# Optimization experiments

Measured on AMD Instinct MI355X. Metric: run time of the kernel, lower is better.

The kernel has to match this reference:

```python
import jax, jax.numpy as jnp
import numpy as np

B, N, C_IN, C_OUT, T, K = 16, 128, 64, 128, 256, 9
PAD = (K - 1) // 2


def conv1d(x, w, b, pad):
    # x: (n, c_in, t), w: (c_out, c_in, k) -> (n, c_out, t)
    y = jax.lax.conv_general_dilated(x, w, (1,), [(pad, pad)],
                                     dimension_numbers=('NCH', 'OIH', 'NCH'))
    return y + b[None, :, None]


def setup_inputs() -> dict:
    key = jax.random.key(0)
    ks = jax.random.split(key, 10)
    xav = lambda k, shape, fan_in, fan_out: jax.random.uniform(
        k, shape, jnp.float32, -1.0, 1.0) * np.sqrt(6.0 / (fan_in + fan_out))
    return {
        'x': jax.random.normal(ks[0], (B, N, C_IN, T), jnp.float32),
        'adjacency': jax.random.uniform(ks[1], (B, N, N), jnp.float32),
        'w_t1': xav(ks[2], (C_OUT, C_IN, K), C_IN * K, C_OUT * K),
        'b_t1': jnp.zeros((C_OUT,), jnp.float32),
        'w_sp': xav(ks[3], (C_OUT, C_OUT), C_OUT, C_OUT),
        'b_sp': jnp.zeros((C_OUT,), jnp.float32),
        'w_t2': xav(ks[4], (C_OUT, C_OUT, K), C_OUT * K, C_OUT * K),
        'b_t2': jnp.zeros((C_OUT,), jnp.float32),
        'w_res': xav(ks[5], (C_OUT, C_IN, 1), C_IN, C_OUT),
        'b_res': jnp.zeros((C_OUT,), jnp.float32),
    }


def reference(x, adjacency, w_t1, b_t1, w_sp, b_sp, w_t2, b_t2, w_res, b_res):
    b, n, c_in, t = x.shape
    xr = x.reshape(b * n, c_in, t)
    # temporal1 + relu
    h = jax.nn.relu(conv1d(xr, w_t1, b_t1, PAD))            # (b*n, c_out, t)
    c_out = h.shape[1]
    h = h.reshape(b, n, c_out, t).transpose(0, 3, 1, 2)      # (b, t, n, c)
    # spatial graph conv, batched over all timesteps at once
    support = jnp.einsum('btnc,co->btno', h, w_sp)
    h = jnp.einsum('bnm,btmo->btno', adjacency, support) + b_sp
    h = jax.nn.relu(h)
    h = h.transpose(0, 2, 3, 1).reshape(b * n, c_out, t)     # (b*n, c, t)
    # temporal2
    h = conv1d(h, w_t2, b_t2, PAD)
    # residual 1x1 conv (in_channels != out_channels)
    res = conv1d(xr, w_res, b_res, 0)
    out = (h + res).reshape(b, n, c_out, t)
    # dropout: identity in eval mode
    return out
```

## Files before the change

kernel.cpp:

```cpp
#include <hip/hip_runtime.h>

#define B_ 16
#define N_ 128
#define CI_ 64
#define CO_ 128
#define T_ 256
#define K_ 9

typedef __attribute__((ext_vector_type(8))) __bf16 bf16x8;
typedef __attribute__((ext_vector_type(4))) float f32x4;
typedef __attribute__((ext_vector_type(8))) unsigned short ushort8;

__device__ __forceinline__ unsigned short tobf(float f) {
  return __builtin_bit_cast(unsigned short, (__bf16)f);
}
__device__ __forceinline__ int swzs(int row, int col0) {
  return ((col0 >> 3) ^ (row & 7)) << 3;
}
__device__ __forceinline__ int swz(int row, int col) {
  return (((col >> 3) ^ (row & 7)) << 3) | (col & 7);
}
#define FRAG(p, idx) (*(const bf16x8*)((p) + (size_t)(idx) * 8))

__device__ __forceinline__ void gload16(const void* g, void* l) {
  __builtin_amdgcn_global_load_lds(
      (const __attribute__((address_space(1))) void*)g,
      (__attribute__((address_space(3))) void*)l, 16, 0, 0);
}

__global__ __launch_bounds__(256) void k_prep(
    const float* __restrict__ w1, const float* __restrict__ w2,
    const float* __restrict__ wsp, const float* __restrict__ wr,
    const float* __restrict__ adj,
    unsigned short* __restrict__ w1f, unsigned short* __restrict__ w2f,
    unsigned short* __restrict__ wrf, unsigned short* __restrict__ wspf,
    unsigned short* __restrict__ adjf) {
  int idx = blockIdx.x * 256 + threadIdx.x;
  int stride = gridDim.x * 256;
  for (int i = idx; i < 73728; i += stride) {
    int e = i & 7, lane = (i >> 3) & 63, ni = (i >> 9) & 3, cg = (i >> 11) & 1;
    int kb = (i >> 12) & 1, k = i >> 13;
    int co = cg * 64 + ni * 16 + (lane & 15), ci = kb * 32 + (lane >> 4) * 8 + e;
    w1f[i] = tobf(w1[(co * 64 + ci) * 9 + k]);
  }
  for (int i = idx; i < 147456; i += stride) {
    int e = i & 7, lane = (i >> 3) & 63, ni = (i >> 9) & 3, cg = (i >> 11) & 1;
    int kb = (i >> 12) & 3, k = i >> 14;
    int co = cg * 64 + ni * 16 + (lane & 15), c = kb * 32 + (lane >> 4) * 8 + e;
    w2f[i] = tobf(w2[(co * 128 + c) * 9 + k]);
  }
  for (int i = idx; i < 8192; i += stride) {
    int e = i & 7, lane = (i >> 3) & 63, ni = (i >> 9) & 3, cg = (i >> 11) & 1;
    int kb = i >> 12;
    int co = cg * 64 + ni * 16 + (lane & 15), ci = kb * 32 + (lane >> 4) * 8 + e;
    wrf[i] = tobf(wr[co * 64 + ci]);
  }
  for (int i = idx; i < 16384; i += stride) {
    int e = i & 7, lane = (i >> 3) & 63, mi = (i >> 9) & 3, og = (i >> 11) & 1;
    int kb = i >> 12;
    int o = og * 64 + mi * 16 + (lane & 15), c = kb * 32 + (lane >> 4) * 8 + e;
    wspf[i] = tobf(wsp[c * 128 + o]);
  }
  for (int i = idx; i < 262144; i += stride) {
    int e = i & 7, lane = (i >> 3) & 63, ni = (i >> 9) & 1, ng = (i >> 10) & 3;
    int kb = (i >> 12) & 3, b = i >> 14;
    int nn = ng * 32 + ni * 16 + (lane & 15), m = kb * 32 + (lane >> 4) * 8 + e;
    adjf[i] = tobf(adj[(b * 128 + nn) * 128 + m]);
  }
}

__global__ __launch_bounds__(256, 4) void k_conv1(
    const float* __restrict__ x, const unsigned short* __restrict__ w1f,
    const float* __restrict__ b1, unsigned short* __restrict__ h1,
    unsigned short* __restrict__ xT) {
  __shared__ alignas(16) char smem[17408];
  unsigned short* xs = (unsigned short*)smem;
  unsigned short* ot = (unsigned short*)smem;

  int tid = threadIdx.x, blk = blockIdx.x;
  int bn = blk >> 1, th = blk & 1, t0 = th * 128;
  const float* xb = x + (size_t)bn * CI_ * T_;
#pragma unroll
  for (int it = 0; it < 8; ++it) {
    int idx = it * 256 + tid;
    int ci = idx >> 5, ch = idx & 31;
    float4 v = *(const float4*)&xb[ci * 256 + t0 + ch * 4];
    int r = 4 + ch * 4;
    xs[(r + 0) * 64 + swz(r + 0, ci)] = tobf(v.x);
    xs[(r + 1) * 64 + swz(r + 1, ci)] = tobf(v.y);
    xs[(r + 2) * 64 + swz(r + 2, ci)] = tobf(v.z);
    xs[(r + 3) * 64 + swz(r + 3, ci)] = tobf(v.w);
  }
  for (int i = tid; i < 512; i += 256) {
    int r8 = i >> 6, ci = i & 63;
    int r = (r8 < 4) ? r8 : 128 + r8;
    int t = t0 - 4 + r;
    float v = (t >= 0 && t < T_) ? xb[ci * 256 + t] : 0.f;
    xs[r * 64 + swz(r, ci)] = tobf(v);
  }

  int lane = tid & 63, wid = tid >> 6;
  int lrow = lane & 15, lk8 = (lane >> 4) * 8, lq = lane >> 4;
  int trow0 = (wid >> 1) * 64, cg = wid & 1;
  const unsigned short* wp = w1f + (size_t)(cg * 256 + lane) * 8;

  f32x4 acc[4][4];
#pragma unroll
  for (int ni = 0; ni < 4; ++ni) {
    float bv = b1[cg * 64 + ni * 16 + lrow];
    f32x4 ini = {bv, bv, bv, bv};
#pragma unroll
    for (int mi = 0; mi < 4; ++mi) acc[mi][ni] = ini;
  }
  __syncthreads();

  {
    unsigned short* xo = xT + ((size_t)bn * T_ + t0) * 64;
    for (int i = tid; i < 1024; i += 256) {
      int tl = i >> 3, s = i & 7;
      int r = tl + 4;
      *(ushort8*)&xo[tl * 64 + s * 8] =
          *(const ushort8*)&xs[r * 64 + ((s ^ (r & 7)) << 3)];
    }
  }

#pragma unroll 2
  for (int it = 0; it < 18; ++it) {
    int k = it >> 1;
    int col0 = (it & 1) * 32 + lk8;
    bf16x8 bfr[4];
#pragma unroll
    for (int ni = 0; ni < 4; ++ni) bfr[ni] = FRAG(wp, it * 512 + ni * 64);
    bf16x8 a[4];
#pragma unroll
    for (int mi = 0; mi < 4; ++mi) {
      int r = trow0 + mi * 16 + lrow + k;
      a[mi] = *(const bf16x8*)&xs[r * 64 + swzs(r, col0)];
    }
#pragma unroll
    for (int mi = 0; mi < 4; ++mi)
#pragma unroll
      for (int ni = 0; ni < 4; ++ni)
        acc[mi][ni] = __builtin_amdgcn_mfma_f32_16x16x32_bf16(
            a[mi], bfr[ni], acc[mi][ni], 0, 0, 0);
  }
  __syncthreads();

  int b = bn >> 7, n = bn & 127;
  for (int ch = 0; ch < 2; ++ch) {
    if ((trow0 >> 6) == ch) {
#pragma unroll
      for (int mi = 0; mi < 4; ++mi)
#pragma unroll
        for (int ni = 0; ni < 4; ++ni) {
          int col = cg * 64 + ni * 16 + lrow;
#pragma unroll
          for (int r = 0; r < 4; ++r) {
            int row = mi * 16 + lq * 4 + r;
            float v = acc[mi][ni][r];
            v = v > 0.f ? v : 0.f;
            ot[row * 128 + swz(row, col)] = tobf(v);
          }
        }
    }
    __syncthreads();
    for (int i = tid; i < 64 * 16; i += 256) {
      int tl = i >> 4, s = i & 15;
      int t = t0 + ch * 64 + tl;
      int ls = s ^ (tl & 7);
      size_t gb = ((size_t)((b * T_ + t) * N_ + n)) << 7;
      *(ushort8*)&h1[gb + ls * 8] = *(const ushort8*)&ot[tl * 128 + s * 8];
    }
    __syncthreads();
  }
}

__global__ __launch_bounds__(512, 4) void k_spatial(
    unsigned short* __restrict__ h1, const unsigned short* __restrict__ adjf,
    const unsigned short* __restrict__ wspf, const float* __restrict__ bsp) {
  __shared__ alignas(16) char smem[65536];
  unsigned short* h1t = (unsigned short*)smem;
  unsigned short* stt = h1t + 16384;
  unsigned short* ot = h1t;

  int tid = threadIdx.x, blk = blockIdx.x;
  int b = blk >> 8;
  unsigned short* h1g = h1 + ((size_t)blk << 14);
#pragma unroll
  for (int it = 0; it < 4; ++it) {
    int i = it * 512 + tid;
    int n = i >> 4, s = i & 15;
    gload16(h1g + n * 128 + ((s ^ (n & 7)) << 3), h1t + ((i & ~63) << 3));
  }
  int lane = tid & 63, wid = tid >> 6;
  int lrow = lane & 15, lk8 = (lane >> 4) * 8, lq = lane >> 4;
  int og = wid >> 2, ng = wid & 3;
  const unsigned short* sp = wspf + (size_t)(og * 256 + lane) * 8;
  const unsigned short* ap = adjf + ((size_t)b * 2048 + ng * 128 + lane) * 8;

  float bspv[4];
#pragma unroll
  for (int oi = 0; oi < 4; ++oi) bspv[oi] = bsp[og * 64 + oi * 16 + lrow];
  __syncthreads();

  f32x4 acc1[4][2];
#pragma unroll
  for (int mi = 0; mi < 4; ++mi)
#pragma unroll
    for (int ni = 0; ni < 2; ++ni) acc1[mi][ni] = (f32x4){0.f, 0.f, 0.f, 0.f};
#pragma unroll
  for (int kb = 0; kb < 4; ++kb) {
    int col0 = kb * 32 + lk8;
    bf16x8 aw[4];
#pragma unroll
    for (int mi = 0; mi < 4; ++mi) aw[mi] = FRAG(sp, kb * 512 + mi * 64);
#pragma unroll
    for (int ni = 0; ni < 2; ++ni) {
      int rn = ng * 32 + ni * 16 + lrow;
      bf16x8 bh = *(const bf16x8*)&h1t[rn * 128 + swzs(rn, col0)];
#pragma unroll
      for (int mi = 0; mi < 4; ++mi)
        acc1[mi][ni] = __builtin_amdgcn_mfma_f32_16x16x32_bf16(
            aw[mi], bh, acc1[mi][ni], 0, 0, 0);
    }
  }
#pragma unroll
  for (int mi = 0; mi < 4; ++mi)
#pragma unroll
    for (int ni = 0; ni < 2; ++ni) {
      int ncol = ng * 32 + ni * 16 + lrow;
#pragma unroll
      for (int r = 0; r < 4; ++r) {
        int o = og * 64 + mi * 16 + lq * 4 + r;
        stt[o * 128 + swz(o, ncol)] = tobf(acc1[mi][ni][r]);
      }
    }
  __syncthreads();

  f32x4 acc2[2][4];
#pragma unroll
  for (int oi = 0; oi < 4; ++oi) {
    f32x4 ini = {bspv[oi], bspv[oi], bspv[oi], bspv[oi]};
#pragma unroll
    for (int ni = 0; ni < 2; ++ni) acc2[ni][oi] = ini;
  }
#pragma unroll
  for (int kb = 0; kb < 4; ++kb) {
    int col0 = kb * 32 + lk8;
    bf16x8 aa[2];
#pragma unroll
    for (int ni = 0; ni < 2; ++ni) aa[ni] = FRAG(ap, kb * 512 + ni * 64);
#pragma unroll
    for (int oi = 0; oi < 4; ++oi) {
      int ro = og * 64 + oi * 16 + lrow;
      bf16x8 bs = *(const bf16x8*)&stt[ro * 128 + swzs(ro, col0)];
#pragma unroll
      for (int ni = 0; ni < 2; ++ni)
        acc2[ni][oi] = __builtin_amdgcn_mfma_f32_16x16x32_bf16(
            aa[ni], bs, acc2[ni][oi], 0, 0, 0);
    }
  }
  __syncthreads();
#pragma unroll
  for (int ni = 0; ni < 2; ++ni)
#pragma unroll
    for (int oi = 0; oi < 4; ++oi) {
      int o = og * 64 + oi * 16 + lrow;
#pragma unroll
      for (int r = 0; r < 4; ++r) {
        int nrow = ng * 32 + ni * 16 + lq * 4 + r;
        float v = acc2[ni][oi][r];
        v = v > 0.f ? v : 0.f;
        ot[nrow * 128 + swz(nrow, o)] = tobf(v);
      }
    }
  __syncthreads();
  for (int i = tid; i < 2048; i += 512) {
    int n = i >> 4, s = i & 15;
    int ls = s ^ (n & 7);
    *(ushort8*)&h1g[n * 128 + ls * 8] = *(const ushort8*)&ot[n * 128 + s * 8];
  }
}

__global__ __launch_bounds__(256, 4) void k_conv2(
    const unsigned short* __restrict__ H2, const unsigned short* __restrict__ xT,
    const unsigned short* __restrict__ w2f, const unsigned short* __restrict__ wrf,
    const float* __restrict__ b2, const float* __restrict__ br,
    float* __restrict__ out) {
  __shared__ alignas(16) char smem[34816];
  unsigned short* h2t = (unsigned short*)smem;
  float* ot = (float*)smem;

  int tid = threadIdx.x, blk = blockIdx.x;
  int bn = blk >> 1, th = blk & 1, t0 = th * 128;
  int b = bn >> 7, n = bn & 127;
  ushort8 zv = {0, 0, 0, 0, 0, 0, 0, 0};
  size_t h2base = ((size_t)(b * T_ + t0 - 4) * N_ + n) << 7;
#pragma unroll
  for (int it = 0; it < 9; ++it) {
    int i = it * 256 + tid;
    if (i < 2176) {
      int tl = i >> 4, s = i & 15;
      int t = t0 - 4 + tl;
      if (t >= 0 && t < T_) {
        gload16(H2 + h2base + (size_t)tl * (N_ * CO_) + ((s ^ (tl & 7)) << 3),
                h2t + ((i & ~63) << 3));
      }
    }
  }
  if (tid < 64) {
    int tl = (th == 0) ? (tid >> 4) : (132 + (tid >> 4));
    int s = tid & 15;
    *(ushort8*)&h2t[tl * 128 + s * 8] = zv;
  }

  int lane = tid & 63, wid = tid >> 6;
  int lrow = lane & 15, lk8 = (lane >> 4) * 8, lq = lane >> 4;
  int trow0 = (wid >> 1) * 64, cg = wid & 1;
  const unsigned short* wpc = w2f + (size_t)(cg * 256 + lane) * 8;
  const unsigned short* rp = wrf + (size_t)(cg * 256 + lane) * 8;

  f32x4 acc[4][4];
#pragma unroll
  for (int ni = 0; ni < 4; ++ni) {
    float bv = b2[cg * 64 + ni * 16 + lrow] + br[cg * 64 + ni * 16 + lrow];
    f32x4 ini = {bv, bv, bv, bv};
#pragma unroll
    for (int mi = 0; mi < 4; ++mi) acc[mi][ni] = ini;
  }
  bf16x8 bA[4], bB[4];
#pragma unroll
  for (int ni = 0; ni < 4; ++ni) bA[ni] = FRAG(wpc, ni * 64);
  __syncthreads();

  for (int it = 0; it < 36; it += 2) {
#pragma unroll
    for (int ni = 0; ni < 4; ++ni) bB[ni] = FRAG(wpc, 512 + ni * 64);
    {
      int k = it >> 2, col0 = (it & 3) * 32 + lk8;
      bf16x8 a[4];
#pragma unroll
      for (int mi = 0; mi < 4; ++mi) {
        int r = trow0 + mi * 16 + lrow + k;
        a[mi] = *(const bf16x8*)&h2t[r * 128 + swzs(r, col0)];
      }
#pragma unroll
      for (int mi = 0; mi < 4; ++mi)
#pragma unroll
        for (int ni = 0; ni < 4; ++ni)
          acc[mi][ni] = __builtin_amdgcn_mfma_f32_16x16x32_bf16(
              a[mi], bA[ni], acc[mi][ni], 0, 0, 0);
    }
    if (it + 2 < 36) {
#pragma unroll
      for (int ni = 0; ni < 4; ++ni) bA[ni] = FRAG(wpc, 1024 + ni * 64);
    }
    {
      int it1 = it + 1;
      int k = it1 >> 2, col0 = (it1 & 3) * 32 + lk8;
      bf16x8 a[4];
#pragma unroll
      for (int mi = 0; mi < 4; ++mi) {
        int r = trow0 + mi * 16 + lrow + k;
        a[mi] = *(const bf16x8*)&h2t[r * 128 + swzs(r, col0)];
      }
#pragma unroll
      for (int mi = 0; mi < 4; ++mi)
#pragma unroll
        for (int ni = 0; ni < 4; ++ni)
          acc[mi][ni] = __builtin_amdgcn_mfma_f32_16x16x32_bf16(
              a[mi], bB[ni], acc[mi][ni], 0, 0, 0);
    }
    wpc += 8192;
  }

  const unsigned short* xg = xT + ((size_t)bn * T_ + t0) * 64;
#pragma unroll
  for (int kb = 0; kb < 2; ++kb) {
    int c0 = kb * 32 + lk8;
    bf16x8 bfr[4];
#pragma unroll
    for (int ni = 0; ni < 4; ++ni) bfr[ni] = FRAG(rp, kb * 512 + ni * 64);
    bf16x8 a[4];
#pragma unroll
    for (int mi = 0; mi < 4; ++mi)
      a[mi] = *(const bf16x8*)&xg[(trow0 + mi * 16 + lrow) * 64 + c0];
#pragma unroll
    for (int mi = 0; mi < 4; ++mi)
#pragma unroll
      for (int ni = 0; ni < 4; ++ni)
        acc[mi][ni] = __builtin_amdgcn_mfma_f32_16x16x32_bf16(
            a[mi], bfr[ni], acc[mi][ni], 0, 0, 0);
  }
  __syncthreads();

  for (int ch = 0; ch < 2; ++ch) {
    if (cg == ch) {
#pragma unroll
      for (int mi = 0; mi < 4; ++mi)
#pragma unroll
        for (int ni = 0; ni < 4; ++ni) {
          int col = ni * 16 + lrow;
          int tl = trow0 + mi * 16 + lq * 4;
          *(f32x4*)&ot[col * 128 + ((((tl >> 2) ^ (col & 7))) << 2)] = acc[mi][ni];
        }
    }
    __syncthreads();
    for (int i = tid; i < 64 * 32; i += 256) {
      int col = i >> 5, s = i & 31;
      float4 v = *(const float4*)&ot[col * 128 + s * 4];
      int lslot = s ^ (col & 7);
      *(float4*)&out[((size_t)bn * 128 + ch * 64 + col) * 256 + t0 + lslot * 4] = v;
    }
    __syncthreads();
  }
}

extern "C" void kernel_launch(void* const* d_in, const int* in_sizes, int n_in,
                              void* d_out, int out_size, void* d_ws, size_t ws_size,
                              hipStream_t stream) {
  const float* x = (const float*)d_in[0];
  const float* adj = (const float*)d_in[1];
  const float* w_t1 = (const float*)d_in[2];
  const float* b_t1 = (const float*)d_in[3];
  const float* w_sp = (const float*)d_in[4];
  const float* b_sp = (const float*)d_in[5];
  const float* w_t2 = (const float*)d_in[6];
  const float* b_t2 = (const float*)d_in[7];
  const float* w_res = (const float*)d_in[8];
  const float* b_res = (const float*)d_in[9];
  float* out = (float*)d_out;

  unsigned short* wsu = (unsigned short*)d_ws;
  unsigned short* h1 = wsu;
  unsigned short* xT = h1 + 67108864;
  unsigned short* w1f = xT + 33554432;
  unsigned short* w2f = w1f + 73728;
  unsigned short* wrf = w2f + 147456;
  unsigned short* wspf = wrf + 8192;
  unsigned short* adjf = wspf + 16384;

  k_prep<<<512, 256, 0, stream>>>(w_t1, w_t2, w_sp, w_res, adj,
                                  w1f, w2f, wrf, wspf, adjf);
  k_conv1<<<B_ * N_ * 2, 256, 0, stream>>>(x, w1f, b_t1, h1, xT);
  k_spatial<<<B_ * T_, 512, 0, stream>>>(h1, adjf, wspf, b_sp);
  k_conv2<<<B_ * N_ * 2, 256, 0, stream>>>(h1, xT, w2f, wrf, b_t2, b_res, out);
}
```

Before: 360.3 us.

## Process full time axis per block in both temporal convolutions

Each conv block now covers all 256 timesteps of one (b,n) row instead of half, doubling the M tile per wave to 8 MFMA row tiles. This removes the halo reloads and halves the weight-fragment traffic per output. conv1 also gains the double-buffered weight prefetch loop already used in conv2. In exchange, LDS and register use per block roughly double, occupancy is lowered to 2 blocks per CU, and the grid shrinks to 2048 blocks.

```diff
diff --git a/kernel.cpp b/kernel.cpp
--- a/kernel.cpp
+++ b/kernel.cpp
@@ -69,22 +69,21 @@
   }
 }
 
-__global__ __launch_bounds__(256, 4) void k_conv1(
+__global__ __launch_bounds__(256, 2) void k_conv1(
     const float* __restrict__ x, const unsigned short* __restrict__ w1f,
     const float* __restrict__ b1, unsigned short* __restrict__ h1,
     unsigned short* __restrict__ xT) {
-  __shared__ alignas(16) char smem[17408];
+  __shared__ alignas(16) char smem[33792];
   unsigned short* xs = (unsigned short*)smem;
   unsigned short* ot = (unsigned short*)smem;
 
-  int tid = threadIdx.x, blk = blockIdx.x;
-  int bn = blk >> 1, th = blk & 1, t0 = th * 128;
+  int tid = threadIdx.x, bn = blockIdx.x;
   const float* xb = x + (size_t)bn * CI_ * T_;
 #pragma unroll
-  for (int it = 0; it < 8; ++it) {
+  for (int it = 0; it < 16; ++it) {
     int idx = it * 256 + tid;
-    int ci = idx >> 5, ch = idx & 31;
-    float4 v = *(const float4*)&xb[ci * 256 + t0 + ch * 4];
+    int ci = idx >> 6, ch = idx & 63;
+    float4 v = *(const float4*)&xb[ci * 256 + ch * 4];
     int r = 4 + ch * 4;
     xs[(r + 0) * 64 + swz(r + 0, ci)] = tobf(v.x);
     xs[(r + 1) * 64 + swz(r + 1, ci)] = tobf(v.y);
@@ -93,30 +92,28 @@
   }
   for (int i = tid; i < 512; i += 256) {
     int r8 = i >> 6, ci = i & 63;
-    int r = (r8 < 4) ? r8 : 128 + r8;
-    int t = t0 - 4 + r;
-    float v = (t >= 0 && t < T_) ? xb[ci * 256 + t] : 0.f;
-    xs[r * 64 + swz(r, ci)] = tobf(v);
+    int r = (r8 < 4) ? r8 : 256 + r8;
+    xs[r * 64 + swz(r, ci)] = 0;
   }
 
   int lane = tid & 63, wid = tid >> 6;
   int lrow = lane & 15, lk8 = (lane >> 4) * 8, lq = lane >> 4;
-  int trow0 = (wid >> 1) * 64, cg = wid & 1;
+  int trow0 = (wid >> 1) * 128, cg = wid & 1;
   const unsigned short* wp = w1f + (size_t)(cg * 256 + lane) * 8;
 
-  f32x4 acc[4][4];
+  f32x4 acc[8][4];
 #pragma unroll
   for (int ni = 0; ni < 4; ++ni) {
     float bv = b1[cg * 64 + ni * 16 + lrow];
     f32x4 ini = {bv, bv, bv, bv};
 #pragma unroll
-    for (int mi = 0; mi < 4; ++mi) acc[mi][ni] = ini;
+    for (int mi = 0; mi < 8; ++mi) acc[mi][ni] = ini;
   }
   __syncthreads();
 
   {
-    unsigned short* xo = xT + ((size_t)bn * T_ + t0) * 64;
-    for (int i = tid; i < 1024; i += 256) {
+    unsigned short* xo = xT + (size_t)bn * T_ * 64;
+    for (int i = tid; i < 2048; i += 256) {
       int tl = i >> 3, s = i & 7;
       int r = tl + 4;
       *(ushort8*)&xo[tl * 64 + s * 8] =
@@ -124,33 +121,56 @@
     }
   }
 
-#pragma unroll 2
-  for (int it = 0; it < 18; ++it) {
-    int k = it >> 1;
-    int col0 = (it & 1) * 32 + lk8;
-    bf16x8 bfr[4];
-#pragma unroll
-    for (int ni = 0; ni < 4; ++ni) bfr[ni] = FRAG(wp, it * 512 + ni * 64);
-    bf16x8 a[4];
-#pragma unroll
-    for (int mi = 0; mi < 4; ++mi) {
-      int r = trow0 + mi * 16 + lrow + k;
-      a[mi] = *(const bf16x8*)&xs[r * 64 + swzs(r, col0)];
-    }
-#pragma unroll
-    for (int mi = 0; mi < 4; ++mi)
-#pragma unroll
-      for (int ni = 0; ni < 4; ++ni)
-        acc[mi][ni] = __builtin_amdgcn_mfma_f32_16x16x32_bf16(
-            a[mi], bfr[ni], acc[mi][ni], 0, 0, 0);
+  bf16x8 bA[4], bB[4];
+#pragma unroll
+  for (int ni = 0; ni < 4; ++ni) bA[ni] = FRAG(wp, ni * 64);
+#pragma unroll 1
+  for (int it = 0; it < 18; it += 2) {
+#pragma unroll
+    for (int ni = 0; ni < 4; ++ni) bB[ni] = FRAG(wp, 512 + ni * 64);
+    {
+      int k = it >> 1, col0 = lk8;
+      bf16x8 a[8];
+#pragma unroll
+      for (int mi = 0; mi < 8; ++mi) {
+        int r = trow0 + mi * 16 + lrow + k;
+        a[mi] = *(const bf16x8*)&xs[r * 64 + swzs(r, col0)];
+      }
+#pragma unroll
+      for (int mi = 0; mi < 8; ++mi)
+#pragma unroll
+        for (int ni = 0; ni < 4; ++ni)
+          acc[mi][ni] = __builtin_amdgcn_mfma_f32_16x16x32_bf16(
+              a[mi], bA[ni], acc[mi][ni], 0, 0, 0);
+    }
+    if (it + 2 < 18) {
+#pragma unroll
+      for (int ni = 0; ni < 4; ++ni) bA[ni] = FRAG(wp, 1024 + ni * 64);
+    }
+    {
+      int k = it >> 1, col0 = 32 + lk8;
+      bf16x8 a[8];
+#pragma unroll
+      for (int mi = 0; mi < 8; ++mi) {
+        int r = trow0 + mi * 16 + lrow + k;
+        a[mi] = *(const bf16x8*)&xs[r * 64 + swzs(r, col0)];
+      }
+#pragma unroll
+      for (int mi = 0; mi < 8; ++mi)
+#pragma unroll
+        for (int ni = 0; ni < 4; ++ni)
+          acc[mi][ni] = __builtin_amdgcn_mfma_f32_16x16x32_bf16(
+              a[mi], bB[ni], acc[mi][ni], 0, 0, 0);
+    }
+    wp += 8192;
   }
   __syncthreads();
 
   int b = bn >> 7, n = bn & 127;
   for (int ch = 0; ch < 2; ++ch) {
-    if ((trow0 >> 6) == ch) {
-#pragma unroll
-      for (int mi = 0; mi < 4; ++mi)
+    if ((trow0 >> 7) == ch) {
+#pragma unroll
+      for (int mi = 0; mi < 8; ++mi)
 #pragma unroll
         for (int ni = 0; ni < 4; ++ni) {
           int col = cg * 64 + ni * 16 + lrow;
@@ -164,9 +184,9 @@
         }
     }
     __syncthreads();
-    for (int i = tid; i < 64 * 16; i += 256) {
+    for (int i = tid; i < 128 * 16; i += 256) {
       int tl = i >> 4, s = i & 15;
-      int t = t0 + ch * 64 + tl;
+      int t = ch * 128 + tl;
       int ls = s ^ (tl & 7);
       size_t gb = ((size_t)((b * T_ + t) * N_ + n)) << 7;
       *(ushort8*)&h1[gb + ls * 8] = *(const ushort8*)&ot[tl * 128 + s * 8];
@@ -282,70 +302,65 @@
   }
 }
 
-__global__ __launch_bounds__(256, 4) void k_conv2(
+__global__ __launch_bounds__(256, 2) void k_conv2(
     const unsigned short* __restrict__ H2, const unsigned short* __restrict__ xT,
     const unsigned short* __restrict__ w2f, const unsigned short* __restrict__ wrf,
     const float* __restrict__ b2, const float* __restrict__ br,
     float* __restrict__ out) {
-  __shared__ alignas(16) char smem[34816];
+  __shared__ alignas(16) char smem[67584];
   unsigned short* h2t = (unsigned short*)smem;
   float* ot = (float*)smem;
 
-  int tid = threadIdx.x, blk = blockIdx.x;
-  int bn = blk >> 1, th = blk & 1, t0 = th * 128;
+  int tid = threadIdx.x, bn = blockIdx.x;
   int b = bn >> 7, n = bn & 127;
   ushort8 zv = {0, 0, 0, 0, 0, 0, 0, 0};
-  size_t h2base = ((size_t)(b * T_ + t0 - 4) * N_ + n) << 7;
-#pragma unroll
-  for (int it = 0; it < 9; ++it) {
+  size_t h2base = ((size_t)(b * T_) * N_ + n) << 7;
+#pragma unroll
+  for (int it = 0; it < 16; ++it) {
     int i = it * 256 + tid;
-    if (i < 2176) {
-      int tl = i >> 4, s = i & 15;
-      int t = t0 - 4 + tl;
-      if (t >= 0 && t < T_) {
-        gload16(H2 + h2base + (size_t)tl * (N_ * CO_) + ((s ^ (tl & 7)) << 3),
-                h2t + ((i & ~63) << 3));
-      }
-    }
-  }
-  if (tid < 64) {
-    int tl = (th == 0) ? (tid >> 4) : (132 + (tid >> 4));
-    int s = tid & 15;
-    *(ushort8*)&h2t[tl * 128 + s * 8] = zv;
+    int t = i >> 4, s = i & 15;
+    gload16(H2 + h2base + (size_t)t * (N_ * CO_) + ((s ^ ((t + 4) & 7)) << 3),
+            h2t + 512 + ((i & ~63) << 3));
+  }
+  if (tid < 128) {
+    int rr = tid >> 4, s = tid & 15;
+    int r = (rr < 4) ? rr : 256 + rr;
+    *(ushort8*)&h2t[r * 128 + s * 8] = zv;
   }
 
   int lane = tid & 63, wid = tid >> 6;
   int lrow = lane & 15, lk8 = (lane >> 4) * 8, lq = lane >> 4;
-  int trow0 = (wid >> 1) * 64, cg = wid & 1;
+  int trow0 = (wid >> 1) * 128, cg = wid & 1;
   const unsigned short* wpc = w2f + (size_t)(cg * 256 + lane) * 8;
   const unsigned short* rp = wrf + (size_t)(cg * 256 + lane) * 8;
 
-  f32x4 acc[4][4];
+  f32x4 acc[8][4];
 #pragma unroll
   for (int ni = 0; ni < 4; ++ni) {
     float bv = b2[cg * 64 + ni * 16 + lrow] + br[cg * 64 + ni * 16 + lrow];
     f32x4 ini = {bv, bv, bv, bv};
 #pragma unroll
-    for (int mi = 0; mi < 4; ++mi) acc[mi][ni] = ini;
+    for (int mi = 0; mi < 8; ++mi) acc[mi][ni] = ini;
   }
   bf16x8 bA[4], bB[4];
 #pragma unroll
   for (int ni = 0; ni < 4; ++ni) bA[ni] = FRAG(wpc, ni * 64);
   __syncthreads();
 
+#pragma unroll 1
   for (int it = 0; it < 36; it += 2) {
 #pragma unroll
     for (int ni = 0; ni < 4; ++ni) bB[ni] = FRAG(wpc, 512 + ni * 64);
     {
       int k = it >> 2, col0 = (it & 3) * 32 + lk8;
-      bf16x8 a[4];
-#pragma unroll
-      for (int mi = 0; mi < 4; ++mi) {
+      bf16x8 a[8];
+#pragma unroll
+      for (int mi = 0; mi < 8; ++mi) {
         int r = trow0 + mi * 16 + lrow + k;
         a[mi] = *(const bf16x8*)&h2t[r * 128 + swzs(r, col0)];
       }
 #pragma unroll
-      for (int mi = 0; mi < 4; ++mi)
+      for (int mi = 0; mi < 8; ++mi)
 #pragma unroll
         for (int ni = 0; ni < 4; ++ni)
           acc[mi][ni] = __builtin_amdgcn_mfma_f32_16x16x32_bf16(
@@ -358,14 +373,14 @@
     {
       int it1 = it + 1;
       int k = it1 >> 2, col0 = (it1 & 3) * 32 + lk8;
-      bf16x8 a[4];
-#pragma unroll
-      for (int mi = 0; mi < 4; ++mi) {
+      bf16x8 a[8];
+#pragma unroll
+      for (int mi = 0; mi < 8; ++mi) {
         int r = trow0 + mi * 16 + lrow + k;
         a[mi] = *(const bf16x8*)&h2t[r * 128 + swzs(r, col0)];
       }
 #pragma unroll
-      for (int mi = 0; mi < 4; ++mi)
+      for (int mi = 0; mi < 8; ++mi)
 #pragma unroll
         for (int ni = 0; ni < 4; ++ni)
           acc[mi][ni] = __builtin_amdgcn_mfma_f32_16x16x32_bf16(
@@ -374,19 +389,19 @@
     wpc += 8192;
   }
 
-  const unsigned short* xg = xT + ((size_t)bn * T_ + t0) * 64;
+  const unsigned short* xg = xT + (size_t)bn * T_ * 64;
 #pragma unroll
   for (int kb = 0; kb < 2; ++kb) {
     int c0 = kb * 32 + lk8;
     bf16x8 bfr[4];
 #pragma unroll
     for (int ni = 0; ni < 4; ++ni) bfr[ni] = FRAG(rp, kb * 512 + ni * 64);
-    bf16x8 a[4];
-#pragma unroll
-    for (int mi = 0; mi < 4; ++mi)
+    bf16x8 a[8];
+#pragma unroll
+    for (int mi = 0; mi < 8; ++mi)
       a[mi] = *(const bf16x8*)&xg[(trow0 + mi * 16 + lrow) * 64 + c0];
 #pragma unroll
-    for (int mi = 0; mi < 4; ++mi)
+    for (int mi = 0; mi < 8; ++mi)
 #pragma unroll
       for (int ni = 0; ni < 4; ++ni)
         acc[mi][ni] = __builtin_amdgcn_mfma_f32_16x16x32_bf16(
@@ -397,20 +412,20 @@
   for (int ch = 0; ch < 2; ++ch) {
     if (cg == ch) {
 #pragma unroll
-      for (int mi = 0; mi < 4; ++mi)
+      for (int mi = 0; mi < 8; ++mi)
 #pragma unroll
         for (int ni = 0; ni < 4; ++ni) {
           int col = ni * 16 + lrow;
           int tl = trow0 + mi * 16 + lq * 4;
-          *(f32x4*)&ot[col * 128 + ((((tl >> 2) ^ (col & 7))) << 2)] = acc[mi][ni];
+          *(f32x4*)&ot[col * 256 + ((((tl >> 2) ^ (col & 7))) << 2)] = acc[mi][ni];
         }
     }
     __syncthreads();
-    for (int i = tid; i < 64 * 32; i += 256) {
-      int col = i >> 5, s = i & 31;
-      float4 v = *(const float4*)&ot[col * 128 + s * 4];
+    for (int i = tid; i < 64 * 64; i += 256) {
+      int col = i >> 6, s = i & 63;
+      float4 v = *(const float4*)&ot[col * 256 + s * 4];
       int lslot = s ^ (col & 7);
-      *(float4*)&out[((size_t)bn * 128 + ch * 64 + col) * 256 + t0 + lslot * 4] = v;
+      *(float4*)&out[((size_t)bn * 128 + ch * 64 + col) * 256 + lslot * 4] = v;
     }
     __syncthreads();
   }
@@ -442,7 +457,7 @@
 
   k_prep<<<512, 256, 0, stream>>>(w_t1, w_t2, w_sp, w_res, adj,
                                   w1f, w2f, wrf, wspf, adjf);
-  k_conv1<<<B_ * N_ * 2, 256, 0, stream>>>(x, w1f, b_t1, h1, xT);
+  k_conv1<<<B_ * N_, 256, 0, stream>>>(x, w1f, b_t1, h1, xT);
   k_spatial<<<B_ * T_, 512, 0, stream>>>(h1, adjf, wspf, b_sp);
-  k_conv2<<<B_ * N_ * 2, 256, 0, stream>>>(h1, xT, w2f, wrf, b_t2, b_res, out);
-}
+  k_conv2<<<B_ * N_, 256, 0, stream>>>(h1, xT, w2f, wrf, b_t2, b_res, out);
+}
```

After: 349.4 us. -3.0%, faster.
